# Kernel tuning notes

Measured on AMD Instinct MI355X. Metric: run time of the kernel, lower is better.

Reference implementation:

```python
import jax, jax.numpy as jnp
import numpy as np

B, N, C, D = 4, 4096, 1024, 32  # batch, tokens, channels, head dim
EPS = 1e-15
PAD_VAL = 1.0


def setup_inputs() -> dict:
    key = jax.random.key(0)
    k1, k2, k3 = jax.random.split(key, 3)
    x = jax.random.normal(k1, (B, N, C), dtype=jnp.float32)
    W_qkv = jax.random.normal(k2, (3 * C, C), dtype=jnp.float32) * 0.02
    W_proj = jax.random.normal(k3, (C, C), dtype=jnp.float32) * 0.02
    b_proj = jnp.zeros((C,), dtype=jnp.float32)
    return {"x": x, "W_qkv": W_qkv, "W_proj": W_proj, "b_proj": b_proj}


def reference(x, W_qkv, W_proj, b_proj):
    Bx, Nx, Cx = x.shape
    h = Cx // D
    # qkv projection (no bias), then split as torch: reshape(B,N,3,C).permute(0,2,3,1)
    qkv = jnp.einsum('bnc,oc->bno', x, W_qkv)            # [B,N,3C]
    qkv = qkv.reshape(Bx, Nx, 3, Cx).transpose(0, 2, 3, 1)  # [B,3,C,N]
    q, k, v = qkv[:, 0], qkv[:, 1], qkv[:, 2]
    q = jax.nn.relu(q.reshape(Bx, h, D, Nx))             # [B,h,D,N]
    k = jax.nn.relu(k.reshape(Bx, h, D, Nx)).transpose(0, 1, 3, 2)  # [B,h,N,D]
    v = v.reshape(Bx, h, D, Nx)                          # [B,h,D,N]
    # pad v with a row of PAD_VAL=1 to carry the normalizer
    v = jnp.concatenate([v, jnp.full((Bx, h, 1, Nx), PAD_VAL, v.dtype)], axis=2)  # [B,h,D+1,N]
    vk = jnp.einsum('bhdn,bhne->bhde', v, k)             # [B,h,D+1,D]
    out = jnp.einsum('bhde,bhen->bhdn', vk, q)           # [B,h,D+1,N]
    out = out[:, :, :-1] / (out[:, :, -1:] + EPS)        # [B,h,D,N]
    out = out.reshape(Bx, Cx, Nx).transpose(0, 2, 1)     # [B,N,C]
    return jnp.einsum('bnc,oc->bno', out, W_proj) + b_proj
```

## Files before the change

kernel.cpp:

```cpp
#include <hip/hip_runtime.h>


using us8   = __attribute__((ext_vector_type(8))) unsigned short;
using us4   = __attribute__((ext_vector_type(4))) unsigned short;
using s8v   = __attribute__((ext_vector_type(8))) short;
using f32x4 = __attribute__((ext_vector_type(4))) float;

__device__ __forceinline__ unsigned short f2bf(float f) {
    union { float f; unsigned int u; } c; c.f = f;
    unsigned int r = c.u + 0x7fffu + ((c.u >> 16) & 1u);
    return (unsigned short)(r >> 16);
}
__device__ __forceinline__ float bf2f(unsigned short u) {
    union { unsigned int u; float f; } c; c.u = ((unsigned int)u) << 16;
    return c.f;
}

__device__ __forceinline__ void async16(const unsigned short* g, unsigned short* l) {
    __builtin_amdgcn_global_load_lds(
        (const __attribute__((address_space(1))) unsigned int*)g,
        (__attribute__((address_space(3))) unsigned int*)l, 16, 0, 0);
}

__global__ __launch_bounds__(256)
void prep(const float* __restrict__ x, const float* __restrict__ wq,
          const float* __restrict__ wp, unsigned short* __restrict__ xb,
          unsigned short* __restrict__ wqb, unsigned short* __restrict__ wpb,
          float* __restrict__ vkws) {
    const int NX = 16777216 / 8, NQ = 3145728 / 8, NP = 1048576 / 8, NZ = 135168 / 8;
    int gid = blockIdx.x * 256 + threadIdx.x;
    const float* in; unsigned short* out; int i;
    if (gid < NX)                    { in = x;  out = xb;  i = gid * 8; }
    else if (gid < NX + NQ)          { in = wq; out = wqb; i = (gid - NX) * 8; }
    else if (gid < NX + NQ + NP)     { in = wp; out = wpb; i = (gid - NX - NQ) * 8; }
    else if (gid < NX + NQ + NP + NZ) {
        int z = (gid - NX - NQ - NP) * 8;
        f32x4 zero = {};
        *(f32x4*)(vkws + z) = zero; *(f32x4*)(vkws + z + 4) = zero;
        return;
    } else return;
    float4 a = *(const float4*)(in + i);
    float4 b = *(const float4*)(in + i + 4);
    us8 o;
    o[0] = f2bf(a.x); o[1] = f2bf(a.y); o[2] = f2bf(a.z); o[3] = f2bf(a.w);
    o[4] = f2bf(b.x); o[5] = f2bf(b.y); o[6] = f2bf(b.z); o[7] = f2bf(b.w);
    *(us8*)(out + i) = o;
}

constexpr int HSZ = 128 * 64;

#define FENCE() asm volatile("" ::: "memory")
#define BARX()  do { FENCE(); __builtin_amdgcn_s_barrier(); FENCE(); } while (0)
#define LGKM0() asm volatile("s_waitcnt lgkmcnt(0)" ::: "memory")

#define MFMA_QUAD(MB, NB)                                                    \
  do {                                                                       \
    __builtin_amdgcn_s_setprio(1);                                           \
    _Pragma("unroll")                                                        \
    for (int mi_ = 0; mi_ < 4; ++mi_)                                        \
      _Pragma("unroll")                                                      \
      for (int ni_ = 0; ni_ < 2; ++ni_)                                      \
        _Pragma("unroll")                                                    \
        for (int kk_ = 0; kk_ < 2; ++kk_)                                    \
          acc[(MB) + mi_][(NB) + ni_] =                                      \
              __builtin_amdgcn_mfma_f32_16x16x32_bf16(                       \
                  af[mi_][kk_], bf[(NB) + ni_][kk_],                         \
                  acc[(MB) + mi_][(NB) + ni_], 0, 0, 0);                     \
    __builtin_amdgcn_s_setprio(0);                                           \
  } while (0)

__device__ __forceinline__
void stage_half(const unsigned short* __restrict__ G, int rowBase, int kcol,
                unsigned short* ldsHalf, int row0, int esw, int wv) {
    async16(G + (size_t)(rowBase + row0) * 1024 + kcol + esw,
            ldsHalf + wv * 512);
    async16(G + (size_t)(rowBase + 64 + row0) * 1024 + kcol + esw,
            ldsHalf + 4096 + wv * 512);
}

template <int MODE>
__device__ __forceinline__
void gemm_core256(const unsigned short* __restrict__ A,
                  const unsigned short* __restrict__ Bt,
                  unsigned short* __restrict__ Cq,
                  unsigned short* __restrict__ kvT,
                  float* __restrict__ Cf, const float* __restrict__ bias,
                  int N, int tM, int tN, unsigned short* lds) {
    unsigned short* As = lds;
    unsigned short* Bs = lds + 4 * HSZ;

    const int t    = threadIdx.x;
    const int lane = t & 63;
    const int wv   = t >> 6;
    const int wr   = wv >> 2;
    const int wc   = wv & 3;
    const int mrow = lane & 15;
    const int kq   = lane >> 4;
    const int m7   = lane & 7;

    const int row0 = t >> 3;
    const int esw  = ((t & 7) ^ (row0 & 7)) * 8;

    const int ks0 = ((0 * 4 + kq) ^ m7) * 8;
    const int ks1 = ((1 * 4 + kq) ^ m7) * 8;
    const int brow = (wc & 1) * 64;

    f32x4 acc[8][4] = {};
    s8v af[4][2], bf[4][2];

    constexpr int NT = 16;

    stage_half(A,  tM,       0,  As + 0 * HSZ, row0, esw, wv);
    stage_half(A,  tM + 128, 0,  As + 1 * HSZ, row0, esw, wv);
    stage_half(Bt, tN,       0,  Bs + 0 * HSZ, row0, esw, wv);
    stage_half(Bt, tN + 128, 0,  Bs + 1 * HSZ, row0, esw, wv);
    stage_half(Bt, tN,       64, Bs + 2 * HSZ, row0, esw, wv);
    stage_half(Bt, tN + 128, 64, Bs + 3 * HSZ, row0, esw, wv);
    stage_half(A,  tM,       64, As + 2 * HSZ, row0, esw, wv);
    asm volatile("s_waitcnt vmcnt(6)" ::: "memory");
    BARX();

    for (int g = 0; g < NT; ++g) {
        const int c = g & 1;
        const unsigned short* Ard = As + (c * 2 + wr) * HSZ;
        const unsigned short* Brd = Bs + (c * 2 + (wc >> 1)) * HSZ;
        const int kt1 = (g + 1 < NT ? g + 1 : NT - 1) * 64;
        const int kt2 = (g + 2 < NT ? g + 2 : NT - 1) * 64;

#pragma unroll
        for (int ni = 0; ni < 2; ++ni) {
            bf[ni][0] = *(const s8v*)&Brd[(brow + ni * 16 + mrow) * 64 + ks0];
            bf[ni][1] = *(const s8v*)&Brd[(brow + ni * 16 + mrow) * 64 + ks1];
        }
#pragma unroll
        for (int mi = 0; mi < 4; ++mi) {
            af[mi][0] = *(const s8v*)&Ard[(mi * 16 + mrow) * 64 + ks0];
            af[mi][1] = *(const s8v*)&Ard[(mi * 16 + mrow) * 64 + ks1];
        }
#pragma unroll
        for (int ni = 2; ni < 4; ++ni) {
            bf[ni][0] = *(const s8v*)&Brd[(brow + ni * 16 + mrow) * 64 + ks0];
            bf[ni][1] = *(const s8v*)&Brd[(brow + ni * 16 + mrow) * 64 + ks1];
        }
        stage_half(A, tM + 128, kt1, As + ((c ^ 1) * 2 + 1) * HSZ, row0, esw, wv);
        MFMA_QUAD(0, 0);
        LGKM0();
        BARX();

        stage_half(Bt, tN, kt2, Bs + (c * 2 + 0) * HSZ, row0, esw, wv);
        MFMA_QUAD(0, 2);
        BARX();

#pragma unroll
        for (int mi = 0; mi < 4; ++mi) {
            af[mi][0] = *(const s8v*)&Ard[(64 + mi * 16 + mrow) * 64 + ks0];
            af[mi][1] = *(const s8v*)&Ard[(64 + mi * 16 + mrow) * 64 + ks1];
        }
        stage_half(Bt, tN + 128, kt2, Bs + (c * 2 + 1) * HSZ, row0, esw, wv);
        MFMA_QUAD(4, 0);
        LGKM0();
        BARX();

        stage_half(A, tM, kt2, As + (c * 2 + 0) * HSZ, row0, esw, wv);
        MFMA_QUAD(4, 2);
        asm volatile("s_waitcnt vmcnt(6)" ::: "memory");
        BARX();
    }

    const int crow0 = kq * 4;
    const int ccol  = mrow;
    if (MODE == 0) {
        if (tN >= 1024) {
            const int b2  = tM >> 12;
            const int nb0 = (tM & 4095) + wr * 128;
#pragma unroll
            for (int mi = 0; mi < 8; ++mi) {
                const int nbase = nb0 + mi * 16 + crow0;
#pragma unroll
                for (int ni = 0; ni < 4; ++ni) {
                    const int col = tN + wc * 64 + ni * 16 + ccol;
                    f32x4 v = acc[mi][ni];
                    if (col < 2048) {
                        v[0] = fmaxf(v[0], 0.f); v[1] = fmaxf(v[1], 0.f);
                        v[2] = fmaxf(v[2], 0.f); v[3] = fmaxf(v[3], 0.f);
                    }
                    us4 o;
                    o[0] = f2bf(v[0]); o[1] = f2bf(v[1]);
                    o[2] = f2bf(v[2]); o[3] = f2bf(v[3]);
                    *(us4*)&kvT[((size_t)b2 * 2048 + (col - 1024)) * 4096 + nbase] = o;
                }
            }
        } else {
#pragma unroll
            for (int mi = 0; mi < 8; ++mi)
#pragma unroll
                for (int ni = 0; ni < 4; ++ni) {
                    const int row = tM + wr * 128 + mi * 16 + crow0;
                    const int col = tN + wc * 64 + ni * 16 + ccol;
#pragma unroll
                    for (int r2 = 0; r2 < 4; ++r2)
                        Cq[(size_t)(row + r2) * 1024 + col] =
                            f2bf(fmaxf(acc[mi][ni][r2], 0.f));
                }
        }
    } else {
#pragma unroll
        for (int mi = 0; mi < 8; ++mi)
#pragma unroll
            for (int ni = 0; ni < 4; ++ni) {
                const int row = tM + wr * 128 + mi * 16 + crow0;
                const int col = tN + wc * 64 + ni * 16 + ccol;
#pragma unroll
                for (int r2 = 0; r2 < 4; ++r2)
                    Cf[(size_t)(row + r2) * N + col] = acc[mi][ni][r2] + bias[col];
            }
    }
    asm volatile("s_waitcnt vmcnt(0)" ::: "memory");
}

__device__ __forceinline__ void xcd_map256(int blk, int MT, int& tM, int& tN) {
    const int xcd = blk & 7;
    const int i   = blk >> 3;
    const int MTx = MT >> 3;
    const int ppan = MTx * 4;
    const int p   = i / ppan;
    const int i2  = i % ppan;
    tM = (xcd * MTx + (i2 >> 2)) * 256;
    tN = (p * 4 + (i2 & 3)) * 256;
}

__global__ __launch_bounds__(512, 2)
void gemm_qkv(const unsigned short* __restrict__ A,
              const unsigned short* __restrict__ Bt,
              unsigned short* __restrict__ Cq, unsigned short* __restrict__ kvT,
              int M, int N) {
    extern __shared__ unsigned short lds[];
    int tM, tN;
    xcd_map256(blockIdx.x, M >> 8, tM, tN);
    gemm_core256<0>(A, Bt, Cq, kvT, nullptr, nullptr, N, tM, tN, lds);
}

__global__ __launch_bounds__(512, 2)
void gemm_proj(const unsigned short* __restrict__ A,
               const unsigned short* __restrict__ Bt,
               float* __restrict__ C, const float* __restrict__ bias,
               int M, int N) {
    extern __shared__ unsigned short lds[];
    int tM, tN;
    xcd_map256(blockIdx.x, M >> 8, tM, tN);
    gemm_core256<1>(A, Bt, nullptr, nullptr, C, bias, N, tM, tN, lds);
}

__global__ __launch_bounds__(256)
void lite_vk(const unsigned short* __restrict__ kvT, float* __restrict__ vkws) {
    const int bh = blockIdx.x, ck = blockIdx.y;
    const int b = bh >> 5, h = bh & 31;
    const int S = 136;
    __shared__ unsigned short Ks[32 * S];
    __shared__ unsigned short Vs[32 * S];
    __shared__ float Rs[4][1088];
    const int t = threadIdx.x, lane = t & 63, wv = t >> 6;
    const unsigned short* Kp = kvT + ((size_t)b * 2048 + h * 32) * 4096 + ck * 512;
    const unsigned short* Vp = kvT + ((size_t)b * 2048 + 1024 + h * 32) * 4096 + ck * 512;
    const int sr = t >> 3, ss = (t & 7) * 16;
    f32x4 acc00 = {}, acc01 = {}, acc10 = {}, acc11 = {}, accO0 = {}, accO1 = {};
    s8v ones;
#pragma unroll
    for (int j = 0; j < 8; ++j) ones[j] = (short)0x3F80;
    const int mrow = lane & 15, kq = (lane >> 4) * 8;

    for (int tile = 0; tile < 4; ++tile) {
        int go = tile * 128 + ss;
        us8 k0v = *(const us8*)(Kp + (size_t)sr * 4096 + go);
        us8 k1v = *(const us8*)(Kp + (size_t)sr * 4096 + go + 8);
        us8 v0v = *(const us8*)(Vp + (size_t)sr * 4096 + go);
        us8 v1v = *(const us8*)(Vp + (size_t)sr * 4096 + go + 8);
        __syncthreads();
        *(us8*)&Ks[sr * S + ss]     = k0v;
        *(us8*)&Ks[sr * S + ss + 8] = k1v;
        *(us8*)&Vs[sr * S + ss]     = v0v;
        *(us8*)&Vs[sr * S + ss + 8] = v1v;
        __syncthreads();
        int ko = wv * 32 + kq;
        s8v a0 = *(const s8v*)&Vs[(mrow)      * S + ko];
        s8v a1 = *(const s8v*)&Vs[(16 + mrow) * S + ko];
        s8v b0 = *(const s8v*)&Ks[(mrow)      * S + ko];
        s8v b1 = *(const s8v*)&Ks[(16 + mrow) * S + ko];
        acc00 = __builtin_amdgcn_mfma_f32_16x16x32_bf16(a0, b0, acc00, 0, 0, 0);
        acc01 = __builtin_amdgcn_mfma_f32_16x16x32_bf16(a0, b1, acc01, 0, 0, 0);
        acc10 = __builtin_amdgcn_mfma_f32_16x16x32_bf16(a1, b0, acc10, 0, 0, 0);
        acc11 = __builtin_amdgcn_mfma_f32_16x16x32_bf16(a1, b1, acc11, 0, 0, 0);
        accO0 = __builtin_amdgcn_mfma_f32_16x16x32_bf16(ones, b0, accO0, 0, 0, 0);
        accO1 = __builtin_amdgcn_mfma_f32_16x16x32_bf16(ones, b1, accO1, 0, 0, 0);
    }

    const int ccol = lane & 15, crow = (lane >> 4) * 4;
    float* R = Rs[wv];
#pragma unroll
    for (int r2 = 0; r2 < 4; ++r2) {
        R[(crow + r2) * 32 + ccol]           = acc00[r2];
        R[(crow + r2) * 32 + 16 + ccol]      = acc01[r2];
        R[(16 + crow + r2) * 32 + ccol]      = acc10[r2];
        R[(16 + crow + r2) * 32 + 16 + ccol] = acc11[r2];
    }
    if ((lane >> 4) == 0) {
        R[1024 + ccol]      = accO0[0];
        R[1024 + 16 + ccol] = accO1[0];
    }
    __syncthreads();
    float* vkb = vkws + bh * (33 * 32);
    for (int i = t; i < 1056; i += 256) {
        float s = Rs[0][i] + Rs[1][i] + Rs[2][i] + Rs[3][i];
        atomicAdd(&vkb[i], s);
    }
}

__global__ __launch_bounds__(256)
void lite_apply(const unsigned short* __restrict__ qb,
                const float* __restrict__ vkws,
                unsigned short* __restrict__ yb) {
    const int bh = blockIdx.x, nb = blockIdx.y;
    const int b = bh >> 5, h = bh & 31;
    __shared__ unsigned short vkh[48 * 32];
    __shared__ unsigned short vkl[48 * 32];
    const int t = threadIdx.x;
    for (int i = t; i < 48 * 32; i += 256) {
        float v = (i < 33 * 32) ? vkws[bh * (33 * 32) + i] : 0.f;
        unsigned short hi = f2bf(v);
        vkh[i] = hi;
        vkl[i] = f2bf(v - bf2f(hi));
    }
    __syncthreads();

    const int lane = t & 63, wv = t >> 6;
    const int col = lane & 15, quad = lane >> 4;
    s8v b0h = *(const s8v*)&vkh[(col)      * 32 + quad * 8];
    s8v b0l = *(const s8v*)&vkl[(col)      * 32 + quad * 8];
    s8v b1h = *(const s8v*)&vkh[(16 + col) * 32 + quad * 8];
    s8v b1l = *(const s8v*)&vkl[(16 + col) * 32 + quad * 8];
    s8v b2h = *(const s8v*)&vkh[(32 + col) * 32 + quad * 8];
    s8v b2l = *(const s8v*)&vkl[(32 + col) * 32 + quad * 8];

    const int ntile = nb * 256 + wv * 64;
#pragma unroll
    for (int mi = 0; mi < 4; ++mi) {
        int tok = ntile + mi * 16 + col;
        const unsigned short* qp =
            qb + (size_t)(b * 4096 + tok) * 1024 + h * 32 + quad * 8;
        s8v a = *(const s8v*)qp;
        f32x4 n0 = {}, n1 = {}, dd = {};
        n0 = __builtin_amdgcn_mfma_f32_16x16x32_bf16(b0h, a, n0, 0, 0, 0);
        n0 = __builtin_amdgcn_mfma_f32_16x16x32_bf16(b0l, a, n0, 0, 0, 0);
        n1 = __builtin_amdgcn_mfma_f32_16x16x32_bf16(b1h, a, n1, 0, 0, 0);
        n1 = __builtin_amdgcn_mfma_f32_16x16x32_bf16(b1l, a, n1, 0, 0, 0);
        dd = __builtin_amdgcn_mfma_f32_16x16x32_bf16(b2h, a, dd, 0, 0, 0);
        dd = __builtin_amdgcn_mfma_f32_16x16x32_bf16(b2l, a, dd, 0, 0, 0);
        float den  = __shfl(dd[0], col, 64);
        float rinv = 1.f / (den + 1e-15f);
        us4 o0, o1;
#pragma unroll
        for (int r = 0; r < 4; ++r) {
            o0[r] = f2bf(n0[r] * rinv);
            o1[r] = f2bf(n1[r] * rinv);
        }
        size_t o = (size_t)(b * 4096 + tok) * 1024 + h * 32;
        *(us4*)&yb[o + quad * 4]      = o0;
        *(us4*)&yb[o + 16 + quad * 4] = o1;
    }
}

extern "C" void kernel_launch(void* const* d_in, const int* in_sizes, int n_in,
                              void* d_out, int out_size, void* d_ws, size_t ws_size,
                              hipStream_t stream) {
    const float* x     = (const float*)d_in[0];
    const float* Wqkv  = (const float*)d_in[1];
    const float* Wproj = (const float*)d_in[2];
    const float* bproj = (const float*)d_in[3];
    float* out = (float*)d_out;

    const int M = 16384, Cdim = 1024, O1 = 3072;

    unsigned short* xb     = (unsigned short*)d_ws;
    unsigned short* wqkvb  = xb + (size_t)M * Cdim;
    unsigned short* wprojb = wqkvb + (size_t)O1 * Cdim;
    unsigned short* qb     = wprojb + (size_t)Cdim * Cdim;
    unsigned short* kvT    = qb + (size_t)M * Cdim;
    unsigned short* ybuf   = kvT + (size_t)4 * 2048 * 4096;
    float* vkws            = (float*)(ybuf + (size_t)M * Cdim);

    static int attr_done = 0;
    if (!attr_done) {
        hipFuncSetAttribute((const void*)gemm_qkv,
                            hipFuncAttributeMaxDynamicSharedMemorySize, 131072);
        hipFuncSetAttribute((const void*)gemm_proj,
                            hipFuncAttributeMaxDynamicSharedMemorySize, 131072);
        attr_done = 1;
    }

    const int PREP_GROUPS = (16777216 + 3145728 + 1048576 + 135168) / 8;
    prep<<<(PREP_GROUPS + 255) / 256, 256, 0, stream>>>(
        x, Wqkv, Wproj, xb, wqkvb, wprojb, vkws);

    gemm_qkv<<<(M / 256) * (O1 / 256), 512, 131072, stream>>>(
        xb, wqkvb, qb, kvT, M, O1);

    lite_vk<<<dim3(128, 8), 256, 0, stream>>>(kvT, vkws);
    lite_apply<<<dim3(128, 16), 256, 0, stream>>>(qb, vkws, ybuf);

    gemm_proj<<<(M / 256) * (Cdim / 256), 512, 131072, stream>>>(
        ybuf, wprojb, out, bproj, M, Cdim);
}
```

Baseline: 311.5 us.

## Remap wave column ownership across B halves and add barriers around MFMA quads

Each wave now owns two 32-column strips, one in each 128-column half of the B tile, instead of one 64-column strip inside a single half. This lets the B fragment loads be split per half so each half can be read right before its MFMA quad, and the epilogue column mapping changes to match. Extra workgroup barriers are inserted before each MFMA quad to order the LDS restaging against the reads. The extra barriers may add synchronisation stalls and reduce overlap between loads and MFMA.

```diff
diff --git a/kernel.cpp b/kernel.cpp
--- a/kernel.cpp
+++ b/kernel.cpp
@@ -103,7 +103,7 @@
 
     const int ks0 = ((0 * 4 + kq) ^ m7) * 8;
     const int ks1 = ((1 * 4 + kq) ^ m7) * 8;
-    const int brow = (wc & 1) * 64;
+    const int browB = wc * 32;
 
     f32x4 acc[8][4] = {};
     s8v af[4][2], bf[4][2];
@@ -122,32 +122,34 @@
 
     for (int g = 0; g < NT; ++g) {
         const int c = g & 1;
-        const unsigned short* Ard = As + (c * 2 + wr) * HSZ;
-        const unsigned short* Brd = Bs + (c * 2 + (wc >> 1)) * HSZ;
+        const unsigned short* Ard  = As + (c * 2 + wr) * HSZ;
+        const unsigned short* B0rd = Bs + (c * 2 + 0) * HSZ;
+        const unsigned short* B1rd = Bs + (c * 2 + 1) * HSZ;
         const int kt1 = (g + 1 < NT ? g + 1 : NT - 1) * 64;
         const int kt2 = (g + 2 < NT ? g + 2 : NT - 1) * 64;
 
-#pragma unroll
-        for (int ni = 0; ni < 2; ++ni) {
-            bf[ni][0] = *(const s8v*)&Brd[(brow + ni * 16 + mrow) * 64 + ks0];
-            bf[ni][1] = *(const s8v*)&Brd[(brow + ni * 16 + mrow) * 64 + ks1];
-        }
+        bf[0][0] = *(const s8v*)&B0rd[(browB + mrow) * 64 + ks0];
+        bf[0][1] = *(const s8v*)&B0rd[(browB + mrow) * 64 + ks1];
+        bf[1][0] = *(const s8v*)&B0rd[(browB + 16 + mrow) * 64 + ks0];
+        bf[1][1] = *(const s8v*)&B0rd[(browB + 16 + mrow) * 64 + ks1];
 #pragma unroll
         for (int mi = 0; mi < 4; ++mi) {
             af[mi][0] = *(const s8v*)&Ard[(mi * 16 + mrow) * 64 + ks0];
             af[mi][1] = *(const s8v*)&Ard[(mi * 16 + mrow) * 64 + ks1];
         }
-#pragma unroll
-        for (int ni = 2; ni < 4; ++ni) {
-            bf[ni][0] = *(const s8v*)&Brd[(brow + ni * 16 + mrow) * 64 + ks0];
-            bf[ni][1] = *(const s8v*)&Brd[(brow + ni * 16 + mrow) * 64 + ks1];
-        }
         stage_half(A, tM + 128, kt1, As + ((c ^ 1) * 2 + 1) * HSZ, row0, esw, wv);
+        BARX();
+        LGKM0();
         MFMA_QUAD(0, 0);
+        BARX();
+
+        bf[2][0] = *(const s8v*)&B1rd[(browB + mrow) * 64 + ks0];
+        bf[2][1] = *(const s8v*)&B1rd[(browB + mrow) * 64 + ks1];
+        bf[3][0] = *(const s8v*)&B1rd[(browB + 16 + mrow) * 64 + ks0];
+        bf[3][1] = *(const s8v*)&B1rd[(browB + 16 + mrow) * 64 + ks1];
+        stage_half(Bt, tN, kt2, Bs + (c * 2 + 0) * HSZ, row0, esw, wv);
+        BARX();
         LGKM0();
-        BARX();
-
-        stage_half(Bt, tN, kt2, Bs + (c * 2 + 0) * HSZ, row0, esw, wv);
         MFMA_QUAD(0, 2);
         BARX();
 
@@ -157,11 +159,13 @@
             af[mi][1] = *(const s8v*)&Ard[(64 + mi * 16 + mrow) * 64 + ks1];
         }
         stage_half(Bt, tN + 128, kt2, Bs + (c * 2 + 1) * HSZ, row0, esw, wv);
+        BARX();
+        LGKM0();
         MFMA_QUAD(4, 0);
-        LGKM0();
         BARX();
 
         stage_half(A, tM, kt2, As + (c * 2 + 0) * HSZ, row0, esw, wv);
+        BARX();
         MFMA_QUAD(4, 2);
         asm volatile("s_waitcnt vmcnt(6)" ::: "memory");
         BARX();
@@ -178,7 +182,7 @@
                 const int nbase = nb0 + mi * 16 + crow0;
 #pragma unroll
                 for (int ni = 0; ni < 4; ++ni) {
-                    const int col = tN + wc * 64 + ni * 16 + ccol;
+                    const int col = tN + (ni >> 1) * 128 + wc * 32 + (ni & 1) * 16 + ccol;
                     f32x4 v = acc[mi][ni];
                     if (col < 2048) {
                         v[0] = fmaxf(v[0], 0.f); v[1] = fmaxf(v[1], 0.f);
@@ -196,7 +200,7 @@
 #pragma unroll
                 for (int ni = 0; ni < 4; ++ni) {
                     const int row = tM + wr * 128 + mi * 16 + crow0;
-                    const int col = tN + wc * 64 + ni * 16 + ccol;
+                    const int col = tN + (ni >> 1) * 128 + wc * 32 + (ni & 1) * 16 + ccol;
 #pragma unroll
                     for (int r2 = 0; r2 < 4; ++r2)
                         Cq[(size_t)(row + r2) * 1024 + col] =
@@ -209,7 +213,7 @@
 #pragma unroll
             for (int ni = 0; ni < 4; ++ni) {
                 const int row = tM + wr * 128 + mi * 16 + crow0;
-                const int col = tN + wc * 64 + ni * 16 + ccol;
+                const int col = tN + (ni >> 1) * 128 + wc * 32 + (ni & 1) * 16 + ccol;
 #pragma unroll
                 for (int r2 = 0; r2 < 4; ++r2)
                     Cf[(size_t)(row + r2) * N + col] = acc[mi][ni][r2] + bias[col];
```

After: 309.8 us. About the same (-0.6%).

## Restructure 256x256 GEMM tiles to four waves with 128x128 per-wave subtiles

Applied to the files above, without the earlier changes.

The two GEMM kernels now run with 256 threads (4 waves) per block instead of 512 (8 waves). Each wave computes a 128x128 output subtile with a 64-entry accumulator array, up from 8x4. The LDS layout changes to split K into 32-wide regions with a new swizzle and per-lane global offset tables, and the k-loop interleaves loads of four regions. The aim is more MFMA work per loaded fragment and fewer LDS reads per MFMA, at the cost of much higher register pressure and one block per CU with fewer waves to hide latency.

```diff
diff --git a/kernel.cpp b/kernel.cpp
--- a/kernel.cpp
+++ b/kernel.cpp
@@ -47,35 +47,31 @@
     *(us8*)(out + i) = o;
 }
 
-constexpr int HSZ = 128 * 64;
+constexpr int RSZ = 8192;
 
 #define FENCE() asm volatile("" ::: "memory")
 #define BARX()  do { FENCE(); __builtin_amdgcn_s_barrier(); FENCE(); } while (0)
 #define LGKM0() asm volatile("s_waitcnt lgkmcnt(0)" ::: "memory")
 
-#define MFMA_QUAD(MB, NB)                                                    \
+#define MFMA_P(AF, NB)                                                       \
   do {                                                                       \
     __builtin_amdgcn_s_setprio(1);                                           \
     _Pragma("unroll")                                                        \
-    for (int mi_ = 0; mi_ < 4; ++mi_)                                        \
+    for (int mi_ = 0; mi_ < 8; ++mi_)                                        \
       _Pragma("unroll")                                                      \
-      for (int ni_ = 0; ni_ < 2; ++ni_)                                      \
-        _Pragma("unroll")                                                    \
-        for (int kk_ = 0; kk_ < 2; ++kk_)                                    \
-          acc[(MB) + mi_][(NB) + ni_] =                                      \
-              __builtin_amdgcn_mfma_f32_16x16x32_bf16(                       \
-                  af[mi_][kk_], bf[(NB) + ni_][kk_],                         \
-                  acc[(MB) + mi_][(NB) + ni_], 0, 0, 0);                     \
+      for (int nj_ = 0; nj_ < 4; ++nj_)                                      \
+        acc[mi_][(NB) + nj_] = __builtin_amdgcn_mfma_f32_16x16x32_bf16(      \
+            AF[mi_], bfr[nj_], acc[mi_][(NB) + nj_], 0, 0, 0);               \
     __builtin_amdgcn_s_setprio(0);                                           \
   } while (0)
 
 __device__ __forceinline__
-void stage_half(const unsigned short* __restrict__ G, int rowBase, int kcol,
-                unsigned short* ldsHalf, int row0, int esw, int wv) {
-    async16(G + (size_t)(rowBase + row0) * 1024 + kcol + esw,
-            ldsHalf + wv * 512);
-    async16(G + (size_t)(rowBase + 64 + row0) * 1024 + kcol + esw,
-            ldsHalf + 4096 + wv * 512);
+void stage_reg(const unsigned short* __restrict__ G, int rowBase, int kcol,
+               unsigned short* region, const int* goff, int wv) {
+#pragma unroll
+    for (int j = 0; j < 4; ++j)
+        async16(G + (size_t)rowBase * 1024 + kcol + goff[j],
+                region + wv * 2048 + j * 512);
 }
 
 template <int MODE>
@@ -87,88 +83,95 @@
                   float* __restrict__ Cf, const float* __restrict__ bias,
                   int N, int tM, int tN, unsigned short* lds) {
     unsigned short* As = lds;
-    unsigned short* Bs = lds + 4 * HSZ;
+    unsigned short* Bs = lds + 4 * RSZ;
 
     const int t    = threadIdx.x;
     const int lane = t & 63;
     const int wv   = t >> 6;
-    const int wr   = wv >> 2;
-    const int wc   = wv & 3;
+    const int wr   = wv >> 1;
+    const int wc   = wv & 1;
     const int mrow = lane & 15;
     const int kq   = lane >> 4;
-    const int m7   = lane & 7;
-
-    const int row0 = t >> 3;
-    const int esw  = ((t & 7) ^ (row0 & 7)) * 8;
-
-    const int ks0 = ((0 * 4 + kq) ^ m7) * 8;
-    const int ks1 = ((1 * 4 + kq) ^ m7) * 8;
-    const int brow = (wc & 1) * 64;
-
-    f32x4 acc[8][4] = {};
-    s8v af[4][2], bf[4][2];
+    const int slot = kq ^ ((mrow >> 1) & 3);
+
+    const int a_off = (wr * 64 + (mrow >> 1)) * 64 + (mrow & 1) * 32 + slot * 8;
+    const int b_off = (wc * 64 + (mrow >> 1)) * 64 + (mrow & 1) * 32 + slot * 8;
+
+    int goff[4];
+#pragma unroll
+    for (int j = 0; j < 4; ++j) {
+        int c   = wv * 256 + j * 64 + lane;
+        int row = ((c >> 3) << 1) + ((c >> 2) & 1);
+        int kqq = (c & 3) ^ ((c >> 3) & 3);
+        goff[j] = row * 1024 + kqq * 8;
+    }
+
+    f32x4 acc[8][8] = {};
+    s8v af0[8], af1[8], bfr[4];
 
     constexpr int NT = 16;
 
-    stage_half(A,  tM,       0,  As + 0 * HSZ, row0, esw, wv);
-    stage_half(A,  tM + 128, 0,  As + 1 * HSZ, row0, esw, wv);
-    stage_half(Bt, tN,       0,  Bs + 0 * HSZ, row0, esw, wv);
-    stage_half(Bt, tN + 128, 0,  Bs + 1 * HSZ, row0, esw, wv);
-    stage_half(Bt, tN,       64, Bs + 2 * HSZ, row0, esw, wv);
-    stage_half(Bt, tN + 128, 64, Bs + 3 * HSZ, row0, esw, wv);
-    stage_half(A,  tM,       64, As + 2 * HSZ, row0, esw, wv);
-    asm volatile("s_waitcnt vmcnt(6)" ::: "memory");
+    stage_reg(A,  tM, 0,       As + 0 * RSZ, goff, wv);
+    stage_reg(A,  tM, 32,      As + 1 * RSZ, goff, wv);
+    stage_reg(Bt, tN, 0,       Bs + 0 * RSZ, goff, wv);
+    stage_reg(Bt, tN, 32,      Bs + 1 * RSZ, goff, wv);
+    stage_reg(A,  tM, 64,      As + 2 * RSZ, goff, wv);
+    stage_reg(Bt, tN, 64,      Bs + 2 * RSZ, goff, wv);
+    stage_reg(A,  tM, 96,      As + 3 * RSZ, goff, wv);
+    asm volatile("s_waitcnt vmcnt(12)" ::: "memory");
     BARX();
 
     for (int g = 0; g < NT; ++g) {
         const int c = g & 1;
-        const unsigned short* Ard = As + (c * 2 + wr) * HSZ;
-        const unsigned short* Brd = Bs + (c * 2 + (wc >> 1)) * HSZ;
+        const unsigned short* A0 = As + (c * 2 + 0) * RSZ;
+        const unsigned short* A1 = As + (c * 2 + 1) * RSZ;
+        const unsigned short* B0 = Bs + (c * 2 + 0) * RSZ;
+        const unsigned short* B1 = Bs + (c * 2 + 1) * RSZ;
         const int kt1 = (g + 1 < NT ? g + 1 : NT - 1) * 64;
         const int kt2 = (g + 2 < NT ? g + 2 : NT - 1) * 64;
 
-#pragma unroll
-        for (int ni = 0; ni < 2; ++ni) {
-            bf[ni][0] = *(const s8v*)&Brd[(brow + ni * 16 + mrow) * 64 + ks0];
-            bf[ni][1] = *(const s8v*)&Brd[(brow + ni * 16 + mrow) * 64 + ks1];
-        }
-#pragma unroll
-        for (int mi = 0; mi < 4; ++mi) {
-            af[mi][0] = *(const s8v*)&Ard[(mi * 16 + mrow) * 64 + ks0];
-            af[mi][1] = *(const s8v*)&Ard[(mi * 16 + mrow) * 64 + ks1];
-        }
-#pragma unroll
-        for (int ni = 2; ni < 4; ++ni) {
-            bf[ni][0] = *(const s8v*)&Brd[(brow + ni * 16 + mrow) * 64 + ks0];
-            bf[ni][1] = *(const s8v*)&Brd[(brow + ni * 16 + mrow) * 64 + ks1];
-        }
-        stage_half(A, tM + 128, kt1, As + ((c ^ 1) * 2 + 1) * HSZ, row0, esw, wv);
-        MFMA_QUAD(0, 0);
+        stage_reg(Bt, tN, kt1 + 32, Bs + ((c ^ 1) * 2 + 1) * RSZ, goff, wv);
+#pragma unroll
+        for (int mi = 0; mi < 8; ++mi)
+            af0[mi] = *(const s8v*)&A0[a_off + mi * 512];
+#pragma unroll
+        for (int nj = 0; nj < 4; ++nj)
+            bfr[nj] = *(const s8v*)&B0[b_off + nj * 512];
+        MFMA_P(af0, 0);
         LGKM0();
         BARX();
 
-        stage_half(Bt, tN, kt2, Bs + (c * 2 + 0) * HSZ, row0, esw, wv);
-        MFMA_QUAD(0, 2);
+        stage_reg(A, tM, kt2, As + (c * 2 + 0) * RSZ, goff, wv);
+#pragma unroll
+        for (int nj = 0; nj < 4; ++nj)
+            bfr[nj] = *(const s8v*)&B0[b_off + (4 + nj) * 512];
+#pragma unroll
+        for (int mi = 0; mi < 8; ++mi)
+            af1[mi] = *(const s8v*)&A1[a_off + mi * 512];
+        MFMA_P(af0, 4);
+        LGKM0();
+        asm volatile("s_waitcnt vmcnt(16)" ::: "memory");
         BARX();
 
-#pragma unroll
-        for (int mi = 0; mi < 4; ++mi) {
-            af[mi][0] = *(const s8v*)&Ard[(64 + mi * 16 + mrow) * 64 + ks0];
-            af[mi][1] = *(const s8v*)&Ard[(64 + mi * 16 + mrow) * 64 + ks1];
-        }
-        stage_half(Bt, tN + 128, kt2, Bs + (c * 2 + 1) * HSZ, row0, esw, wv);
-        MFMA_QUAD(4, 0);
+        stage_reg(Bt, tN, kt2, Bs + (c * 2 + 0) * RSZ, goff, wv);
+#pragma unroll
+        for (int nj = 0; nj < 4; ++nj)
+            bfr[nj] = *(const s8v*)&B1[b_off + nj * 512];
+        MFMA_P(af1, 0);
         LGKM0();
         BARX();
 
-        stage_half(A, tM, kt2, As + (c * 2 + 0) * HSZ, row0, esw, wv);
-        MFMA_QUAD(4, 2);
-        asm volatile("s_waitcnt vmcnt(6)" ::: "memory");
+        stage_reg(A, tM, kt2 + 32, As + (c * 2 + 1) * RSZ, goff, wv);
+#pragma unroll
+        for (int nj = 0; nj < 4; ++nj)
+            bfr[nj] = *(const s8v*)&B1[b_off + (4 + nj) * 512];
+        MFMA_P(af1, 4);
+        LGKM0();
+        asm volatile("s_waitcnt vmcnt(16)" ::: "memory");
         BARX();
     }
 
     const int crow0 = kq * 4;
-    const int ccol  = mrow;
     if (MODE == 0) {
         if (tN >= 1024) {
             const int b2  = tM >> 12;
@@ -177,8 +180,8 @@
             for (int mi = 0; mi < 8; ++mi) {
                 const int nbase = nb0 + mi * 16 + crow0;
 #pragma unroll
-                for (int ni = 0; ni < 4; ++ni) {
-                    const int col = tN + wc * 64 + ni * 16 + ccol;
+                for (int ni = 0; ni < 8; ++ni) {
+                    const int col = tN + wc * 128 + ni * 16 + mrow;
                     f32x4 v = acc[mi][ni];
                     if (col < 2048) {
                         v[0] = fmaxf(v[0], 0.f); v[1] = fmaxf(v[1], 0.f);
@@ -194,9 +197,9 @@
 #pragma unroll
             for (int mi = 0; mi < 8; ++mi)
 #pragma unroll
-                for (int ni = 0; ni < 4; ++ni) {
+                for (int ni = 0; ni < 8; ++ni) {
                     const int row = tM + wr * 128 + mi * 16 + crow0;
-                    const int col = tN + wc * 64 + ni * 16 + ccol;
+                    const int col = tN + wc * 128 + ni * 16 + mrow;
 #pragma unroll
                     for (int r2 = 0; r2 < 4; ++r2)
                         Cq[(size_t)(row + r2) * 1024 + col] =
@@ -207,9 +210,9 @@
 #pragma unroll
         for (int mi = 0; mi < 8; ++mi)
 #pragma unroll
-            for (int ni = 0; ni < 4; ++ni) {
+            for (int ni = 0; ni < 8; ++ni) {
                 const int row = tM + wr * 128 + mi * 16 + crow0;
-                const int col = tN + wc * 64 + ni * 16 + ccol;
+                const int col = tN + wc * 128 + ni * 16 + mrow;
 #pragma unroll
                 for (int r2 = 0; r2 < 4; ++r2)
                     Cf[(size_t)(row + r2) * N + col] = acc[mi][ni][r2] + bias[col];
@@ -229,7 +232,7 @@
     tN = (p * 4 + (i2 & 3)) * 256;
 }
 
-__global__ __launch_bounds__(512, 2)
+__global__ __launch_bounds__(256, 1)
 void gemm_qkv(const unsigned short* __restrict__ A,
               const unsigned short* __restrict__ Bt,
               unsigned short* __restrict__ Cq, unsigned short* __restrict__ kvT,
@@ -240,7 +243,7 @@
     gemm_core256<0>(A, Bt, Cq, kvT, nullptr, nullptr, N, tM, tN, lds);
 }
 
-__global__ __launch_bounds__(512, 2)
+__global__ __launch_bounds__(256, 1)
 void gemm_proj(const unsigned short* __restrict__ A,
                const unsigned short* __restrict__ Bt,
                float* __restrict__ C, const float* __restrict__ bias,
@@ -401,12 +404,12 @@
     prep<<<(PREP_GROUPS + 255) / 256, 256, 0, stream>>>(
         x, Wqkv, Wproj, xb, wqkvb, wprojb, vkws);
 
-    gemm_qkv<<<(M / 256) * (O1 / 256), 512, 131072, stream>>>(
+    gemm_qkv<<<(M / 256) * (O1 / 256), 256, 131072, stream>>>(
         xb, wqkvb, qb, kvT, M, O1);
 
     lite_vk<<<dim3(128, 8), 256, 0, stream>>>(kvT, vkws);
     lite_apply<<<dim3(128, 16), 256, 0, stream>>>(qb, vkws, ybuf);
 
-    gemm_proj<<<(M / 256) * (Cdim / 256), 512, 131072, stream>>>(
+    gemm_proj<<<(M / 256) * (Cdim / 256), 256, 131072, stream>>>(
         ybuf, wprojb, out, bproj, M, Cdim);
 }
```

New measurement: 318.4 us. +2.2%, slower.

## Load B fragments directly from global into registers, triple-buffer A in LDS

Applied to the files above, without the earlier changes.

Reworks the shared GEMM main loop so that B operand fragments are read straight from global memory into double-buffered registers, one tile ahead. Only A is staged through LDS, now with a three-stage rotating buffer and one barrier per k-tile instead of four. LDS use per block drops from 128 KB to 96 KB. The cost is uncoalesced-ish per-lane global loads for B with no LDS reuse across waves, plus higher register pressure from two B fragment sets.

```diff
diff --git a/kernel.cpp b/kernel.cpp
--- a/kernel.cpp
+++ b/kernel.cpp
@@ -47,36 +47,65 @@
     *(us8*)(out + i) = o;
 }
 
-constexpr int HSZ = 128 * 64;
-
 #define FENCE() asm volatile("" ::: "memory")
 #define BARX()  do { FENCE(); __builtin_amdgcn_s_barrier(); FENCE(); } while (0)
-#define LGKM0() asm volatile("s_waitcnt lgkmcnt(0)" ::: "memory")
-
-#define MFMA_QUAD(MB, NB)                                                    \
+
+#define MFMA_H(AF, BF, MB)                                                   \
   do {                                                                       \
     __builtin_amdgcn_s_setprio(1);                                           \
     _Pragma("unroll")                                                        \
     for (int mi_ = 0; mi_ < 4; ++mi_)                                        \
       _Pragma("unroll")                                                      \
-      for (int ni_ = 0; ni_ < 2; ++ni_)                                      \
+      for (int ni_ = 0; ni_ < 4; ++ni_)                                      \
         _Pragma("unroll")                                                    \
         for (int kk_ = 0; kk_ < 2; ++kk_)                                    \
-          acc[(MB) + mi_][(NB) + ni_] =                                      \
-              __builtin_amdgcn_mfma_f32_16x16x32_bf16(                       \
-                  af[mi_][kk_], bf[(NB) + ni_][kk_],                         \
-                  acc[(MB) + mi_][(NB) + ni_], 0, 0, 0);                     \
+          acc[(MB) + mi_][ni_] = __builtin_amdgcn_mfma_f32_16x16x32_bf16(    \
+              AF[mi_][kk_], BF[ni_][kk_], acc[(MB) + mi_][ni_], 0, 0, 0);    \
     __builtin_amdgcn_s_setprio(0);                                           \
   } while (0)
 
-__device__ __forceinline__
-void stage_half(const unsigned short* __restrict__ G, int rowBase, int kcol,
-                unsigned short* ldsHalf, int row0, int esw, int wv) {
-    async16(G + (size_t)(rowBase + row0) * 1024 + kcol + esw,
-            ldsHalf + wv * 512);
-    async16(G + (size_t)(rowBase + 64 + row0) * 1024 + kcol + esw,
-            ldsHalf + 4096 + wv * 512);
-}
+#define GATHERB(DST, KT)                                                     \
+  do {                                                                       \
+    _Pragma("unroll")                                                        \
+    for (int ni_ = 0; ni_ < 4; ++ni_) {                                      \
+      DST[ni_][0] = *(const s8v*)(Bgl + (size_t)ni_ * 16384 + (KT));         \
+      DST[ni_][1] = *(const s8v*)(Bgl + (size_t)ni_ * 16384 + (KT) + 32);    \
+    }                                                                        \
+  } while (0)
+
+#define STAGEA(KT, BUF)                                                      \
+  do {                                                                       \
+    _Pragma("unroll")                                                        \
+    for (int j_ = 0; j_ < 4; ++j_)                                           \
+      async16(Aglane + (size_t)j_ * 65536 + (KT),                            \
+              (BUF) + j_ * 4096 + wv * 512);                                 \
+  } while (0)
+
+#define TILEG(G, BUSE, BPRE)                                                 \
+  do {                                                                       \
+    unsigned short* bufR = lds + 16384 * ((G) % 3);                          \
+    unsigned short* bufS = lds + 16384 * (((G) + 2) % 3);                    \
+    const int ktB = ((G) + 1 < 16 ? (G) + 1 : 15) * 64;                      \
+    const int ktA = ((G) + 2 < 16 ? (G) + 2 : 15) * 64;                      \
+    _Pragma("unroll")                                                        \
+    for (int mi_ = 0; mi_ < 4; ++mi_) {                                      \
+      af[mi_][0] = *(const s8v*)&bufR[(wr * 128 + mi_ * 16 + mrow) * 64 + ks0]; \
+      af[mi_][1] = *(const s8v*)&bufR[(wr * 128 + mi_ * 16 + mrow) * 64 + ks1]; \
+    }                                                                        \
+    GATHERB(BPRE, ktB);                                                      \
+    FENCE();                                                                 \
+    MFMA_H(af, BUSE, 0);                                                     \
+    STAGEA(ktA, bufS);                                                       \
+    FENCE();                                                                 \
+    _Pragma("unroll")                                                        \
+    for (int mi_ = 0; mi_ < 4; ++mi_) {                                      \
+      af[mi_][0] = *(const s8v*)&bufR[(wr * 128 + 64 + mi_ * 16 + mrow) * 64 + ks0]; \
+      af[mi_][1] = *(const s8v*)&bufR[(wr * 128 + 64 + mi_ * 16 + mrow) * 64 + ks1]; \
+    }                                                                        \
+    MFMA_H(af, BUSE, 4);                                                     \
+    asm volatile("s_waitcnt vmcnt(12)" ::: "memory");                        \
+    BARX();                                                                  \
+  } while (0)
 
 template <int MODE>
 __device__ __forceinline__
@@ -86,9 +115,6 @@
                   unsigned short* __restrict__ kvT,
                   float* __restrict__ Cf, const float* __restrict__ bias,
                   int N, int tM, int tN, unsigned short* lds) {
-    unsigned short* As = lds;
-    unsigned short* Bs = lds + 4 * HSZ;
-
     const int t    = threadIdx.x;
     const int lane = t & 63;
     const int wv   = t >> 6;
@@ -100,71 +126,28 @@
 
     const int row0 = t >> 3;
     const int esw  = ((t & 7) ^ (row0 & 7)) * 8;
+    const unsigned short* Aglane = A + (size_t)(tM + row0) * 1024 + esw;
+
+    const unsigned short* Bgl =
+        Bt + (size_t)(tN + wc * 64 + mrow) * 1024 + kq * 8;
 
     const int ks0 = ((0 * 4 + kq) ^ m7) * 8;
     const int ks1 = ((1 * 4 + kq) ^ m7) * 8;
-    const int brow = (wc & 1) * 64;
 
     f32x4 acc[8][4] = {};
-    s8v af[4][2], bf[4][2];
-
-    constexpr int NT = 16;
-
-    stage_half(A,  tM,       0,  As + 0 * HSZ, row0, esw, wv);
-    stage_half(A,  tM + 128, 0,  As + 1 * HSZ, row0, esw, wv);
-    stage_half(Bt, tN,       0,  Bs + 0 * HSZ, row0, esw, wv);
-    stage_half(Bt, tN + 128, 0,  Bs + 1 * HSZ, row0, esw, wv);
-    stage_half(Bt, tN,       64, Bs + 2 * HSZ, row0, esw, wv);
-    stage_half(Bt, tN + 128, 64, Bs + 3 * HSZ, row0, esw, wv);
-    stage_half(A,  tM,       64, As + 2 * HSZ, row0, esw, wv);
-    asm volatile("s_waitcnt vmcnt(6)" ::: "memory");
+    s8v af[4][2], bA[4][2], bB[4][2];
+
+    STAGEA(0, lds);
+    STAGEA(64, lds + 16384);
+    FENCE();
+    GATHERB(bA, 0);
+    asm volatile("s_waitcnt vmcnt(12)" ::: "memory");
     BARX();
 
-    for (int g = 0; g < NT; ++g) {
-        const int c = g & 1;
-        const unsigned short* Ard = As + (c * 2 + wr) * HSZ;
-        const unsigned short* Brd = Bs + (c * 2 + (wc >> 1)) * HSZ;
-        const int kt1 = (g + 1 < NT ? g + 1 : NT - 1) * 64;
-        const int kt2 = (g + 2 < NT ? g + 2 : NT - 1) * 64;
-
-#pragma unroll
-        for (int ni = 0; ni < 2; ++ni) {
-            bf[ni][0] = *(const s8v*)&Brd[(brow + ni * 16 + mrow) * 64 + ks0];
-            bf[ni][1] = *(const s8v*)&Brd[(brow + ni * 16 + mrow) * 64 + ks1];
-        }
-#pragma unroll
-        for (int mi = 0; mi < 4; ++mi) {
-            af[mi][0] = *(const s8v*)&Ard[(mi * 16 + mrow) * 64 + ks0];
-            af[mi][1] = *(const s8v*)&Ard[(mi * 16 + mrow) * 64 + ks1];
-        }
-#pragma unroll
-        for (int ni = 2; ni < 4; ++ni) {
-            bf[ni][0] = *(const s8v*)&Brd[(brow + ni * 16 + mrow) * 64 + ks0];
-            bf[ni][1] = *(const s8v*)&Brd[(brow + ni * 16 + mrow) * 64 + ks1];
-        }
-        stage_half(A, tM + 128, kt1, As + ((c ^ 1) * 2 + 1) * HSZ, row0, esw, wv);
-        MFMA_QUAD(0, 0);
-        LGKM0();
-        BARX();
-
-        stage_half(Bt, tN, kt2, Bs + (c * 2 + 0) * HSZ, row0, esw, wv);
-        MFMA_QUAD(0, 2);
-        BARX();
-
-#pragma unroll
-        for (int mi = 0; mi < 4; ++mi) {
-            af[mi][0] = *(const s8v*)&Ard[(64 + mi * 16 + mrow) * 64 + ks0];
-            af[mi][1] = *(const s8v*)&Ard[(64 + mi * 16 + mrow) * 64 + ks1];
-        }
-        stage_half(Bt, tN + 128, kt2, Bs + (c * 2 + 1) * HSZ, row0, esw, wv);
-        MFMA_QUAD(4, 0);
-        LGKM0();
-        BARX();
-
-        stage_half(A, tM, kt2, As + (c * 2 + 0) * HSZ, row0, esw, wv);
-        MFMA_QUAD(4, 2);
-        asm volatile("s_waitcnt vmcnt(6)" ::: "memory");
-        BARX();
+#pragma unroll
+    for (int g2 = 0; g2 < 8; ++g2) {
+        TILEG(2 * g2,     bA, bB);
+        TILEG(2 * g2 + 1, bB, bA);
     }
 
     const int crow0 = kq * 4;
@@ -391,9 +374,9 @@
     static int attr_done = 0;
     if (!attr_done) {
         hipFuncSetAttribute((const void*)gemm_qkv,
-                            hipFuncAttributeMaxDynamicSharedMemorySize, 131072);
+                            hipFuncAttributeMaxDynamicSharedMemorySize, 98304);
         hipFuncSetAttribute((const void*)gemm_proj,
-                            hipFuncAttributeMaxDynamicSharedMemorySize, 131072);
+                            hipFuncAttributeMaxDynamicSharedMemorySize, 98304);
         attr_done = 1;
     }
 
@@ -401,12 +384,12 @@
     prep<<<(PREP_GROUPS + 255) / 256, 256, 0, stream>>>(
         x, Wqkv, Wproj, xb, wqkvb, wprojb, vkws);
 
-    gemm_qkv<<<(M / 256) * (O1 / 256), 512, 131072, stream>>>(
+    gemm_qkv<<<(M / 256) * (O1 / 256), 512, 98304, stream>>>(
         xb, wqkvb, qb, kvT, M, O1);
 
     lite_vk<<<dim3(128, 8), 256, 0, stream>>>(kvT, vkws);
     lite_apply<<<dim3(128, 16), 256, 0, stream>>>(qb, vkws, ybuf);
 
-    gemm_proj<<<(M / 256) * (Cdim / 256), 512, 131072, stream>>>(
+    gemm_proj<<<(M / 256) * (Cdim / 256), 512, 98304, stream>>>(
         ybuf, wprojb, out, bproj, M, Cdim);
 }
```

Result: slower. 358.3 us (+15.0%).
